# Optimization experiments

Measured on AMD Instinct MI355X. Metric: run time of the kernel, lower is better.

## Reference

```python
import jax, jax.numpy as jnp
from jax import lax
import numpy as np

B = 65536


def setup_inputs() -> dict:
    key = jax.random.key(0)
    ks = jax.random.split(key, 7)
    return {
        "x": jax.random.normal(ks[0], (B, 1, 28, 28), dtype=jnp.float32),
        "W1": jax.random.normal(ks[1], (8, 1, 3, 3), dtype=jnp.float32) * 0.3,
        "b1": jax.random.normal(ks[2], (8,), dtype=jnp.float32) * 0.1,
        "W2": jax.random.normal(ks[3], (16, 8, 3, 3), dtype=jnp.float32) * 0.1,
        "b2": jax.random.normal(ks[4], (16,), dtype=jnp.float32) * 0.1,
        "Wfc": jax.random.normal(ks[5], (1, 784), dtype=jnp.float32) * 0.03,
        "bfc": jax.random.normal(ks[6], (1,), dtype=jnp.float32) * 0.1,
    }


def _conv(x, w, b):
    # NCHW / OIHW, stride 2, padding 1 (matches nn.Conv2d(kernel=3, stride=2, padding=1))
    y = lax.conv_general_dilated(x, w, window_strides=(2, 2), padding=((1, 1), (1, 1)))
    return y + b[None, :, None, None]


def reference(x, W1, b1, W2, b2, Wfc, bfc):
    z = jax.nn.relu(_conv(x, W1, b1))            # [B,8,14,14]
    z = jax.nn.relu(_conv(z, W2, b2))            # [B,16,7,7]
    z = z.reshape(z.shape[0], -1)                # [B,784], channel-major like torch flatten
    rates = jax.nn.softplus(z @ Wfc.T + bfc) + 0.001   # [B,1]
    rates = rates[:, 0]                          # [B]
    # Logistic ODE du/dt = -k*u, u(0)=1 over t in [0,1] -> u(1) = exp(-k)
    probs = 1.0 - jnp.exp(-rates)
    return jnp.clip(probs, 1e-6, 1.0 - 1e-6)
```

## Files before the change

### kernel.cpp

```cpp
#include <hip/hip_runtime.h>
#include <math.h>


typedef short bf16x8 __attribute__((ext_vector_type(8)));
typedef float f32x4  __attribute__((ext_vector_type(4)));

#define NBLOCKS 4096
#define Z1_RS 19
#define Z1_SLOTS (15 * Z1_RS)
#define IMG_RS 36
#define IMG_ROWS 29
#define IMG_FLOATS (IMG_ROWS * IMG_RS)

static __device__ __forceinline__ short f2bf(float f) {
    union { float f; unsigned u; } v; v.f = f;
    unsigned r = v.u + 0x7FFF + ((v.u >> 16) & 1);
    return (short)(r >> 16);
}

#define CONV1_PAIR(CA, PKDST) do {                                          \
    const float* wa_ = &W1[(CA) * 9];                                       \
    const float* wc_ = &W1[((CA) + 1) * 9];                                 \
    float za_ = b1[(CA)], zc_ = b1[(CA) + 1];                               \
    za_ = fmaf(t0, wa_[0], za_); zc_ = fmaf(t0, wc_[0], zc_);               \
    za_ = fmaf(t1, wa_[1], za_); zc_ = fmaf(t1, wc_[1], zc_);               \
    za_ = fmaf(t2, wa_[2], za_); zc_ = fmaf(t2, wc_[2], zc_);               \
    za_ = fmaf(t3, wa_[3], za_); zc_ = fmaf(t3, wc_[3], zc_);               \
    za_ = fmaf(t4, wa_[4], za_); zc_ = fmaf(t4, wc_[4], zc_);               \
    za_ = fmaf(t5, wa_[5], za_); zc_ = fmaf(t5, wc_[5], zc_);               \
    za_ = fmaf(t6, wa_[6], za_); zc_ = fmaf(t6, wc_[6], zc_);               \
    za_ = fmaf(t7, wa_[7], za_); zc_ = fmaf(t7, wc_[7], zc_);               \
    za_ = fmaf(t8, wa_[8], za_); zc_ = fmaf(t8, wc_[8], zc_);               \
    za_ = fmaxf(za_, 0.f);       zc_ = fmaxf(zc_, 0.f);                     \
    asm("v_cvt_pk_bf16_f32 %0, %1, %2" : "=v"(PKDST) : "v"(za_), "v"(zc_)); \
} while (0)

#define CONV1_STEP(WBOFF, ZOFF, STORE_COND) do {                              \
    const float* wbse = sw + (WBOFF);                                         \
    float t0 = wbse[0],            t1 = wbse[1],              t2 = wbse[2];   \
    float t3 = wbse[IMG_RS],       t4 = wbse[IMG_RS + 1],     t5 = wbse[IMG_RS + 2]; \
    float t6 = wbse[2 * IMG_RS],   t7 = wbse[2 * IMG_RS + 1], t8 = wbse[2 * IMG_RS + 2]; \
    asm volatile("" : "+v"(t0), "+v"(t1), "+v"(t2), "+v"(t3), "+v"(t4),      \
                      "+v"(t5), "+v"(t6), "+v"(t7), "+v"(t8));                \
    unsigned pk0_, pk1_, pk2_, pk3_;                                          \
    CONV1_PAIR(0, pk0_);                                                      \
    CONV1_PAIR(2, pk1_);                                                      \
    CONV1_PAIR(4, pk2_);                                                      \
    CONV1_PAIR(6, pk3_);                                                      \
    if (STORE_COND)                                                           \
        *(uint4*)(z1b + (ZOFF)) = make_uint4(pk0_, pk1_, pk2_, pk3_);         \
} while (0)

__global__ __launch_bounds__(256, 4) void fused_cnn_mfma(
    const float* __restrict__ x,
    const float* __restrict__ W1, const float* __restrict__ b1,
    const float* __restrict__ W2, const float* __restrict__ b2,
    const float* __restrict__ Wfc, const float* __restrict__ bfc,
    float* __restrict__ out, int nimg)
{
    __shared__ __align__(16) float simg[4][IMG_FLOATS];
    __shared__ bf16x8 sz1[4][Z1_SLOTS];

    const int tid  = threadIdx.x;
    const int w    = tid >> 6;
    const int lane = tid & 63;
    const int hi   = lane >> 4;
    const int lo   = lane & 15;

    {
        f32x4 z4 = {0.f, 0.f, 0.f, 0.f};
        f32x4* sp = (f32x4*)&simg[w][0];
        for (int i = lane; i < IMG_FLOATS / 4; i += 64) sp[i] = z4;
        bf16x8 zz = {0,0,0,0,0,0,0,0};
        for (int i = lane; i < Z1_SLOTS; i += 64) sz1[w][i] = zz;
    }

    #define MK_WB(KK) ({                                                    \
        bf16x8 v_;                                                          \
        const int tap_ = (KK) * 4 + hi;                                     \
        _Pragma("unroll")                                                   \
        for (int j = 0; j < 8; j++)                                         \
            v_[j] = (tap_ < 9) ? f2bf(W2[lo * 72 + j * 9 + tap_])           \
                               : (short)0;                                  \
        v_; })
    const bf16x8 wb0 = MK_WB(0), wb1 = MK_WB(1), wb2 = MK_WB(2);

    #define MK_POSOFF(T) ({                                                 \
        int p_ = (T) * 16 + lo; if (p_ > 48) p_ = 48;                       \
        int qy_ = p_ / 7, qx_ = p_ - qy_ * 7;                               \
        ((2 * qy_) * Z1_RS + 2 * qx_) * 16; })
    const int posoff0 = MK_POSOFF(0), posoff1 = MK_POSOFF(1),
              posoff2 = MK_POSOFF(2), posoff3 = MK_POSOFF(3);
    #define MK_TAPOFF(KK) ({                                                \
        int tap_ = (KK) * 4 + hi;                                           \
        int ty_ = tap_ / 3, tx_ = tap_ - ty_ * 3;                           \
        (tap_ < 9) ? (ty_ * Z1_RS + tx_) * 16 : 0; })
    const int tapoff0 = MK_TAPOFF(0), tapoff1 = MK_TAPOFF(1),
              tapoff2 = MK_TAPOFF(2);

    #define MK_SRC4(J) ({ int p4_ = (J) * 64 + lane;                        \
                          if (p4_ > 195) p4_ = 195; p4_; })
    const int src40 = MK_SRC4(0), src41 = MK_SRC4(1),
              src42 = MK_SRC4(2), src43 = MK_SRC4(3);
    #define MK_DSTF(J) ({                                                   \
        int p4_ = (J) * 64 + lane; if (p4_ > 195) p4_ = 195;                \
        int yy_ = p4_ / 7, xq_ = p4_ - yy_ * 7;                             \
        (yy_ + 1) * IMG_RS + 4 + 4 * xq_; })
    const int dstf0 = MK_DSTF(0), dstf1 = MK_DSTF(1),
              dstf2 = MK_DSTF(2), dstf3 = MK_DSTF(3);

    #define MK_WBOFF(I) ({                                                  \
        int p_ = (I) * 64 + lane; if (p_ > 195) p_ = 195;                   \
        int py_ = p_ / 14, px_ = p_ - py_ * 14;                             \
        (2 * py_) * IMG_RS + 2 * px_ + 3; })
    const int wboff0 = MK_WBOFF(0), wboff1 = MK_WBOFF(1),
              wboff2 = MK_WBOFF(2), wboff3 = MK_WBOFF(3);
    #define MK_ZOFF(I) ({                                                   \
        int p_ = (I) * 64 + lane; if (p_ > 195) p_ = 195;                   \
        int py_ = p_ / 14, px_ = p_ - py_ * 14;                             \
        ((py_ + 1) * Z1_RS + px_ + 1) * 16; })
    const int zoff0 = MK_ZOFF(0), zoff1 = MK_ZOFF(1),
              zoff2 = MK_ZOFF(2), zoff3 = MK_ZOFF(3);

    const float b2v = b2[lo];
    #define MK_WFC(T) ({                                                    \
        f32x4 v_;                                                           \
        _Pragma("unroll")                                                   \
        for (int r = 0; r < 4; r++) {                                       \
            int p_ = (T) * 16 + hi * 4 + r;                                 \
            v_[r] = (p_ < 49) ? Wfc[lo * 49 + p_] : 0.f;                    \
        }                                                                   \
        v_; })
    const f32x4 wfct0 = MK_WFC(0), wfct1 = MK_WFC(1),
                wfct2 = MK_WFC(2), wfct3 = MK_WFC(3);
    const float bfc0 = bfc[0];

    const int nquad = (nimg + 3) >> 2;
    float* const sw = &simg[w][0];
    char* const z1b = (char*)&sz1[w][0];

    float4 pf0, pf1, pf2, pf3;
    {
        int img = blockIdx.x * 4 + w;
        if (img >= nimg) img = nimg - 1;
        const float4* sp = (const float4*)(x + (size_t)img * 784);
        pf0 = sp[src40]; pf1 = sp[src41]; pf2 = sp[src42]; pf3 = sp[src43];
    }

    for (int q = blockIdx.x; q < nquad; q += gridDim.x) {
        *(float4*)(sw + dstf0) = pf0;
        *(float4*)(sw + dstf1) = pf1;
        *(float4*)(sw + dstf2) = pf2;
        if (lane < 4) *(float4*)(sw + dstf3) = pf3;

        {
            int qn = q + gridDim.x;
            if (qn < nquad) {
                int imgn = qn * 4 + w;
                if (imgn >= nimg) imgn = nimg - 1;
                const float4* sp = (const float4*)(x + (size_t)imgn * 784);
                pf0 = sp[src40]; pf1 = sp[src41];
                pf2 = sp[src42]; pf3 = sp[src43];
            }
        }

        CONV1_STEP(wboff0, zoff0, 1);
        CONV1_STEP(wboff1, zoff1, 1);
        CONV1_STEP(wboff2, zoff2, 1);
        CONV1_STEP(wboff3, zoff3, lane < 4);

        f32x4 acc0 = {0.f, 0.f, 0.f, 0.f};
        f32x4 acc1 = {0.f, 0.f, 0.f, 0.f};
        f32x4 acc2 = {0.f, 0.f, 0.f, 0.f};
        f32x4 acc3 = {0.f, 0.f, 0.f, 0.f};
        #define C2(ACC, POS) do {                                           \
            ACC = __builtin_amdgcn_mfma_f32_16x16x32_bf16(                  \
                *(const bf16x8*)(z1b + (POS) + tapoff0), wb0, ACC, 0, 0, 0);\
            ACC = __builtin_amdgcn_mfma_f32_16x16x32_bf16(                  \
                *(const bf16x8*)(z1b + (POS) + tapoff1), wb1, ACC, 0, 0, 0);\
            ACC = __builtin_amdgcn_mfma_f32_16x16x32_bf16(                  \
                *(const bf16x8*)(z1b + (POS) + tapoff2), wb2, ACC, 0, 0, 0);\
        } while (0)
        C2(acc0, posoff0);
        C2(acc1, posoff1);
        C2(acc2, posoff2);
        C2(acc3, posoff3);

        float fc = 0.f;
        #define EPI(ACC, WF) do {                                           \
            _Pragma("unroll")                                               \
            for (int r = 0; r < 4; r++) {                                   \
                float z_ = fmaxf((ACC)[r] + b2v, 0.f);                      \
                fc = fmaf(z_, (WF)[r], fc);                                 \
            }                                                               \
        } while (0)
        EPI(acc0, wfct0);
        EPI(acc1, wfct1);
        EPI(acc2, wfct2);
        EPI(acc3, wfct3);
        #pragma unroll
        for (int off = 32; off > 0; off >>= 1)
            fc += __shfl_down(fc, off, 64);

        if (lane == 0) {
            int img = q * 4 + w;
            if (img < nimg) {
                float v    = fc + bfc0;
                float sp   = fmaxf(v, 0.f) + log1pf(expf(-fabsf(v)));
                float rate = sp + 0.001f;
                float pr   = 1.f - expf(-rate);
                out[img] = fminf(fmaxf(pr, 1e-6f), 1.f - 1e-6f);
            }
        }
    }
}

extern "C" void kernel_launch(void* const* d_in, const int* in_sizes, int n_in,
                              void* d_out, int out_size, void* d_ws, size_t ws_size,
                              hipStream_t stream) {
    const float* x   = (const float*)d_in[0];
    const float* W1  = (const float*)d_in[1];
    const float* b1  = (const float*)d_in[2];
    const float* W2  = (const float*)d_in[3];
    const float* b2  = (const float*)d_in[4];
    const float* Wfc = (const float*)d_in[5];
    const float* bfc = (const float*)d_in[6];
    float* out = (float*)d_out;

    const int nimg  = in_sizes[0] / 784;
    const int nquad = (nimg + 3) / 4;
    const int grid  = nquad < NBLOCKS ? nquad : NBLOCKS;

    fused_cnn_mfma<<<grid, 256, 0, stream>>>(x, W1, b1, W2, b2, Wfc, bfc,
                                             out, nimg);
}
```

Before: 316.5 us.

## Read conv1 inputs directly from global memory, dropping LDS image staging

```diff
diff --git a/kernel.cpp b/kernel.cpp
--- a/kernel.cpp
+++ b/kernel.cpp
@@ -8,9 +8,6 @@
 #define NBLOCKS 4096
 #define Z1_RS 19
 #define Z1_SLOTS (15 * Z1_RS)
-#define IMG_RS 36
-#define IMG_ROWS 29
-#define IMG_FLOATS (IMG_ROWS * IMG_RS)
 
 static __device__ __forceinline__ short f2bf(float f) {
     union { float f; unsigned u; } v; v.f = f;
@@ -35,30 +32,45 @@
     asm("v_cvt_pk_bf16_f32 %0, %1, %2" : "=v"(PKDST) : "v"(za_), "v"(zc_)); \
 } while (0)
 
-#define CONV1_STEP(WBOFF, ZOFF, STORE_COND) do {                              \
-    const float* wbse = sw + (WBOFF);                                         \
-    float t0 = wbse[0],            t1 = wbse[1],              t2 = wbse[2];   \
-    float t3 = wbse[IMG_RS],       t4 = wbse[IMG_RS + 1],     t5 = wbse[IMG_RS + 2]; \
-    float t6 = wbse[2 * IMG_RS],   t7 = wbse[2 * IMG_RS + 1], t8 = wbse[2 * IMG_RS + 2]; \
-    asm volatile("" : "+v"(t0), "+v"(t1), "+v"(t2), "+v"(t3), "+v"(t4),      \
+#define CONV1_STEP(I, STORE_COND) do {                                        \
+    int p_ = (I) * 64 + lane; if (p_ > 195) p_ = 195;                         \
+    int py_ = p_ / 14, px_ = p_ - py_ * 14;                                   \
+    int r1_ = py_ * 56;                                       \
+    int r0_ = r1_ - 28; if (r0_ < 0) r0_ = 0;                                 \
+    int r2_ = r1_ + 28;                                                       \
+    int c1_ = px_ * 2;                                                        \
+    int c0_ = c1_ - 1; if (c0_ < 0) c0_ = 0;                                  \
+    float mt_  = (py_ > 0) ? 1.f : 0.f;                                       \
+    float ml_  = (px_ > 0) ? 1.f : 0.f;                                       \
+    float mtl_ = mt_ * ml_;                                                   \
+    float2 a12 = *(const float2*)(xi + r0_ + c1_);            \
+    float  a0  = xi[r0_ + c0_];                                               \
+    float2 b45 = *(const float2*)(xi + r1_ + c1_);                            \
+    float  b3  = xi[r1_ + c0_];                                               \
+    float2 c78 = *(const float2*)(xi + r2_ + c1_);                            \
+    float  c6  = xi[r2_ + c0_];                                               \
+    float t0 = a0 * mtl_, t1 = a12.x * mt_, t2 = a12.y * mt_;                 \
+    float t3 = b3 * ml_,  t4 = b45.x,       t5 = b45.y;                       \
+    float t6 = c6 * ml_,  t7 = c78.x,       t8 = c78.y;                       \
+    asm volatile("" : "+v"(t0), "+v"(t1), "+v"(t2), "+v"(t3), "+v"(t4),       \
                       "+v"(t5), "+v"(t6), "+v"(t7), "+v"(t8));                \
     unsigned pk0_, pk1_, pk2_, pk3_;                                          \
     CONV1_PAIR(0, pk0_);                                                      \
     CONV1_PAIR(2, pk1_);                                                      \
     CONV1_PAIR(4, pk2_);                                                      \
     CONV1_PAIR(6, pk3_);                                                      \
+    int zoff_ = ((py_ + 1) * Z1_RS + px_ + 1) * 16;                           \
     if (STORE_COND)                                                           \
-        *(uint4*)(z1b + (ZOFF)) = make_uint4(pk0_, pk1_, pk2_, pk3_);         \
+        *(uint4*)(z1b + zoff_) = make_uint4(pk0_, pk1_, pk2_, pk3_);          \
 } while (0)
 
-__global__ __launch_bounds__(256, 4) void fused_cnn_mfma(
+__global__ __launch_bounds__(256, 6) void fused_cnn_mfma(
     const float* __restrict__ x,
     const float* __restrict__ W1, const float* __restrict__ b1,
     const float* __restrict__ W2, const float* __restrict__ b2,
     const float* __restrict__ Wfc, const float* __restrict__ bfc,
     float* __restrict__ out, int nimg)
 {
-    __shared__ __align__(16) float simg[4][IMG_FLOATS];
     __shared__ bf16x8 sz1[4][Z1_SLOTS];
 
     const int tid  = threadIdx.x;
@@ -68,9 +80,6 @@
     const int lo   = lane & 15;
 
     {
-        f32x4 z4 = {0.f, 0.f, 0.f, 0.f};
-        f32x4* sp = (f32x4*)&simg[w][0];
-        for (int i = lane; i < IMG_FLOATS / 4; i += 64) sp[i] = z4;
         bf16x8 zz = {0,0,0,0,0,0,0,0};
         for (int i = lane; i < Z1_SLOTS; i += 64) sz1[w][i] = zz;
     }
@@ -98,30 +107,6 @@
     const int tapoff0 = MK_TAPOFF(0), tapoff1 = MK_TAPOFF(1),
               tapoff2 = MK_TAPOFF(2);
 
-    #define MK_SRC4(J) ({ int p4_ = (J) * 64 + lane;                        \
-                          if (p4_ > 195) p4_ = 195; p4_; })
-    const int src40 = MK_SRC4(0), src41 = MK_SRC4(1),
-              src42 = MK_SRC4(2), src43 = MK_SRC4(3);
-    #define MK_DSTF(J) ({                                                   \
-        int p4_ = (J) * 64 + lane; if (p4_ > 195) p4_ = 195;                \
-        int yy_ = p4_ / 7, xq_ = p4_ - yy_ * 7;                             \
-        (yy_ + 1) * IMG_RS + 4 + 4 * xq_; })
-    const int dstf0 = MK_DSTF(0), dstf1 = MK_DSTF(1),
-              dstf2 = MK_DSTF(2), dstf3 = MK_DSTF(3);
-
-    #define MK_WBOFF(I) ({                                                  \
-        int p_ = (I) * 64 + lane; if (p_ > 195) p_ = 195;                   \
-        int py_ = p_ / 14, px_ = p_ - py_ * 14;                             \
-        (2 * py_) * IMG_RS + 2 * px_ + 3; })
-    const int wboff0 = MK_WBOFF(0), wboff1 = MK_WBOFF(1),
-              wboff2 = MK_WBOFF(2), wboff3 = MK_WBOFF(3);
-    #define MK_ZOFF(I) ({                                                   \
-        int p_ = (I) * 64 + lane; if (p_ > 195) p_ = 195;                   \
-        int py_ = p_ / 14, px_ = p_ - py_ * 14;                             \
-        ((py_ + 1) * Z1_RS + px_ + 1) * 16; })
-    const int zoff0 = MK_ZOFF(0), zoff1 = MK_ZOFF(1),
-              zoff2 = MK_ZOFF(2), zoff3 = MK_ZOFF(3);
-
     const float b2v = b2[lo];
     #define MK_WFC(T) ({                                                    \
         f32x4 v_;                                                           \
@@ -136,38 +121,17 @@
     const float bfc0 = bfc[0];
 
     const int nquad = (nimg + 3) >> 2;
-    float* const sw = &simg[w][0];
     char* const z1b = (char*)&sz1[w][0];
 
-    float4 pf0, pf1, pf2, pf3;
-    {
-        int img = blockIdx.x * 4 + w;
+    for (int q = blockIdx.x; q < nquad; q += gridDim.x) {
+        int img = q * 4 + w;
         if (img >= nimg) img = nimg - 1;
-        const float4* sp = (const float4*)(x + (size_t)img * 784);
-        pf0 = sp[src40]; pf1 = sp[src41]; pf2 = sp[src42]; pf3 = sp[src43];
-    }
-
-    for (int q = blockIdx.x; q < nquad; q += gridDim.x) {
-        *(float4*)(sw + dstf0) = pf0;
-        *(float4*)(sw + dstf1) = pf1;
-        *(float4*)(sw + dstf2) = pf2;
-        if (lane < 4) *(float4*)(sw + dstf3) = pf3;
-
-        {
-            int qn = q + gridDim.x;
-            if (qn < nquad) {
-                int imgn = qn * 4 + w;
-                if (imgn >= nimg) imgn = nimg - 1;
-                const float4* sp = (const float4*)(x + (size_t)imgn * 784);
-                pf0 = sp[src40]; pf1 = sp[src41];
-                pf2 = sp[src42]; pf3 = sp[src43];
-            }
-        }
-
-        CONV1_STEP(wboff0, zoff0, 1);
-        CONV1_STEP(wboff1, zoff1, 1);
-        CONV1_STEP(wboff2, zoff2, 1);
-        CONV1_STEP(wboff3, zoff3, lane < 4);
+        const float* __restrict__ xi = x + (size_t)img * 784;
+
+        CONV1_STEP(0, 1);
+        CONV1_STEP(1, 1);
+        CONV1_STEP(2, 1);
+        CONV1_STEP(3, lane < 4);
 
         f32x4 acc0 = {0.f, 0.f, 0.f, 0.f};
         f32x4 acc1 = {0.f, 0.f, 0.f, 0.f};
@@ -203,13 +167,13 @@
             fc += __shfl_down(fc, off, 64);
 
         if (lane == 0) {
-            int img = q * 4 + w;
-            if (img < nimg) {
+            int imgo = q * 4 + w;
+            if (imgo < nimg) {
                 float v    = fc + bfc0;
                 float sp   = fmaxf(v, 0.f) + log1pf(expf(-fabsf(v)));
                 float rate = sp + 0.001f;
                 float pr   = 1.f - expf(-rate);
-                out[img] = fminf(fmaxf(pr, 1e-6f), 1.f - 1e-6f);
+                out[imgo] = fminf(fmaxf(pr, 1e-6f), 1.f - 1e-6f);
             }
         }
     }
```

Result: slower. 533.5 us (+68.5%).
